# Kernel optimization log

Hardware: AMD Instinct MI355X
Metric: run time of the kernel (lower is better)

Reference implementation:

```python
import jax, jax.numpy as jnp
import numpy as np

H = 512
V = 50000
S = 400
B = 64


def setup_inputs() -> dict:
    key = jax.random.key(0)
    ks = jax.random.split(key, 20)
    inp = {
        'input': jax.random.normal(ks[0], (1, B, H), jnp.float32),
        'encoder_states': jax.random.normal(ks[1], (S, B, H), jnp.float32),
        'oov_enc_mask': jax.random.randint(ks[2], (S, B), 0, 2, jnp.int32),
        'hidden': jnp.zeros((1, B, H), jnp.float32),
        # GRU params (PyTorch layout: gates ordered r, z, n)
        'W_ih': jax.random.normal(ks[3], (3 * H, H), jnp.float32) * 0.02,
        'W_hh': jax.random.normal(ks[4], (3 * H, H), jnp.float32) * 0.02,
        'b_ih': jax.random.normal(ks[5], (3 * H,), jnp.float32) * 0.02,
        'b_hh': jax.random.normal(ks[6], (3 * H,), jnp.float32) * 0.02,
        # output vocab projection Linear(2H, V)
        'out_W': jax.random.normal(ks[7], (V, 2 * H), jnp.float32) * 0.02,
        'out_b': jax.random.normal(ks[8], (V,), jnp.float32) * 0.02,
        # additive attention params
        'v': jax.random.normal(ks[9], (H, 1), jnp.float32) * 0.02,
        'Wh': jax.random.normal(ks[10], (H, H), jnp.float32) * 0.02,
        'Ws': jax.random.normal(ks[11], (H, H), jnp.float32) * 0.02,
        'b_attn': jax.random.normal(ks[12], (1, H), jnp.float32) * 0.02,
        # pointer probability Linears (H -> 1)
        'pWh': jax.random.normal(ks[13], (1, H), jnp.float32) * 0.02,
        'pWs': jax.random.normal(ks[14], (1, H), jnp.float32) * 0.02,
        'pWx': jax.random.normal(ks[15], (1, H), jnp.float32) * 0.02,
        'pWx_b': jax.random.normal(ks[16], (1,), jnp.float32) * 0.02,
    }
    return inp


def reference(input, encoder_states, oov_enc_mask, hidden,
              W_ih, W_hh, b_ih, b_hh, out_W, out_b,
              v, Wh, Ws, b_attn, pWh, pWs, pWx, pWx_b):
    x = input[0]            # (B, H)
    h0 = hidden[0]          # (B, H)

    # --- single-step GRU (PyTorch gate order r, z, n) ---
    gi = x @ W_ih.T + b_ih      # (B, 3H)
    gh = h0 @ W_hh.T + b_hh     # (B, 3H)
    ir, iz, inn = jnp.split(gi, 3, axis=1)
    hr, hz, hn = jnp.split(gh, 3, axis=1)
    r = jax.nn.sigmoid(ir + hr)
    z = jax.nn.sigmoid(iz + hz)
    n = jnp.tanh(inn + r * hn)
    h = (1.0 - z) * n + z * h0          # decoder_state, (B, H)
    hidden_new = h[None]                # (1, B, H)

    # --- Bahdanau additive attention, softmax over seq axis ---
    x1 = jnp.einsum('sbh,hk->sbk', encoder_states, Wh)   # (S, B, H)
    x2 = h @ Ws                                          # (B, H) broadcasts over S
    scores = jnp.squeeze(jnp.tanh(x1 + x2 + b_attn) @ v, 2)  # (S, B)
    attn = jax.nn.softmax(scores, axis=0)                # (S, B)
    attn_bs = attn.T                                     # (B, S)

    context = jnp.einsum('bs,sbh->bh', attn_bs, encoder_states)  # (B, H)
    global_state = jnp.concatenate([h, context], axis=1)         # (B, 2H)

    # --- pointer probability ---
    p = jax.nn.sigmoid(context @ pWh.T + h @ pWs.T + x @ pWx.T + pWx_b)  # (B, 1)

    vocab_distr = p * jax.nn.selu(global_state @ out_W.T + out_b)        # (B, V)
    oov_vocab_distr = (1.0 - p) * (attn_bs * oov_enc_mask.astype(jnp.float32).T)  # (B, S)
    extended_vocab_distr = jnp.concatenate([vocab_distr, oov_vocab_distr], axis=1)

    return extended_vocab_distr, hidden_new, jnp.squeeze(p), attn
```

## Files before the change

kernel.cpp:

```cpp
#include <hip/hip_runtime.h>
#include <cmath>

#define H    512
#define H2   1024
#define V    50000
#define SEQ  400
#define EXT  (V + SEQ)
#define NB_V 782

typedef __attribute__((ext_vector_type(8))) short short8;
typedef __attribute__((ext_vector_type(4))) float floatx4;

__device__ __forceinline__ unsigned int bfpack2(float lo, float hi) {
    unsigned int a = __float_as_uint(lo) + 0x8000u;
    unsigned int b = __float_as_uint(hi) + 0x8000u;
    return __builtin_amdgcn_perm(b, a, 0x07060302);
}
__device__ __forceinline__ uint4 pack8(float4 a, float4 b) {
    uint4 r;
    r.x = bfpack2(a.x, a.y);
    r.y = bfpack2(a.z, a.w);
    r.z = bfpack2(b.x, b.y);
    r.w = bfpack2(b.z, b.w);
    return r;
}
__device__ __forceinline__ float4 ld4(const float* p) { return *(const float4*)p; }

__global__ __launch_bounds__(256) void k01_fused(
    const float* __restrict__ x, const float* __restrict__ h0,
    const float* __restrict__ W_ih, const float* __restrict__ W_hh,
    float* __restrict__ gacc,
    const float* __restrict__ Wh, const float* __restrict__ Ws,
    unsigned short* __restrict__ WhT, unsigned short* __restrict__ WsT)
{
    __shared__ __align__(16) unsigned char smem[65536];
    const int tid = threadIdx.x;

    if (blockIdx.x >= 64) {
        float (*T)[65] = (float (*)[65])smem;
        const int e   = blockIdx.x - 64;
        const int zz  = e >> 6, rem = e & 63;
        const int k0  = (rem & 7) * 64, n0 = (rem >> 3) * 64;
        const float* src = zz ? Ws : Wh;
        unsigned short* dst = zz ? WsT : WhT;
        #pragma unroll
        for (int i = 0; i < 16; ++i) {
            int ee = i * 256 + tid;
            int r = ee >> 6, c = ee & 63;
            T[r][c] = src[(size_t)(k0 + r) * H + n0 + c];
        }
        __syncthreads();
        #pragma unroll
        for (int i = 0; i < 16; ++i) {
            int ee = i * 256 + tid;
            int nn = ee >> 6, kk = ee & 63;
            unsigned int u = __float_as_uint(T[kk][nn]) + 0x8000u;
            dst[(size_t)(n0 + nn) * H + k0 + kk] = (unsigned short)(u >> 16);
        }
        return;
    }

    uint4* Ax = (uint4*)smem;
    uint4* Ah = (uint4*)(smem + 8192);
    uint4 (*Bg)[512] = (uint4 (*)[512])(smem + 16384);
    const int wave = tid >> 6, lane = tid & 63;
    const int lrow = lane & 15, q = lane >> 4;
    const int jb = blockIdx.x & 7, ks = blockIdx.x >> 3;
    const int J0 = jb * 64;
    const int kc = ks * 64;

    #pragma unroll
    for (int c = 0; c < 2; ++c) {
        int idx = c * 256 + tid;
        int m = idx >> 3, j2 = idx & 7, k8 = j2 ^ (m & 7);
        const float* sx = x  + m * H + kc + k8 * 8;
        const float* sh = h0 + m * H + kc + k8 * 8;
        Ax[idx] = pack8(ld4(sx), ld4(sx + 4));
        Ah[idx] = pack8(ld4(sh), ld4(sh + 4));
    }
    #pragma unroll
    for (int g = 0; g < 6; ++g) {
        const float* Wb = (g < 3) ? W_ih : W_hh;
        const int go = (g % 3) * H;
        #pragma unroll
        for (int c = 0; c < 2; ++c) {
            int idx = c * 256 + tid;
            int n = idx >> 3, j2 = idx & 7, k8 = j2 ^ (n & 7);
            const float* sw = Wb + (size_t)(go + J0 + n) * H + kc + k8 * 8;
            Bg[g][idx] = pack8(ld4(sw), ld4(sw + 4));
        }
    }
    __syncthreads();

    floatx4 accm[6][4];
    #pragma unroll
    for (int g = 0; g < 6; ++g)
        #pragma unroll
        for (int mt = 0; mt < 4; ++mt) accm[g][mt] = (floatx4){0.f, 0.f, 0.f, 0.f};

    #pragma unroll
    for (int kk8 = 0; kk8 < 8; kk8 += 4) {
        const int k8 = kk8 + q;
        short8 ax[4], ah[4];
        #pragma unroll
        for (int mt = 0; mt < 4; ++mt) {
            int m = mt * 16 + lrow;
            ax[mt] = *(const short8*)&Ax[m * 8 + (k8 ^ (m & 7))];
            ah[mt] = *(const short8*)&Ah[m * 8 + (k8 ^ (m & 7))];
        }
        const int n = wave * 16 + lrow;
        const int gidx = n * 8 + (k8 ^ (n & 7));
        #pragma unroll
        for (int g = 0; g < 6; ++g) {
            short8 bb = *(const short8*)&Bg[g][gidx];
            #pragma unroll
            for (int mt = 0; mt < 4; ++mt)
                accm[g][mt] = __builtin_amdgcn_mfma_f32_16x16x32_bf16(
                    (g < 3) ? ax[mt] : ah[mt], bb, accm[g][mt], 0, 0, 0);
        }
    }
    const int j = J0 + wave * 16 + lrow;
    #pragma unroll
    for (int g = 0; g < 6; ++g)
        #pragma unroll
        for (int mt = 0; mt < 4; ++mt)
            #pragma unroll
            for (int r = 0; r < 4; ++r) {
                const int bb = mt * 16 + q * 4 + r;
                gacc[(((size_t)g * 8 + ks) * 64 + bb) * H + j] = accm[g][mt][r];
            }
}

__global__ __launch_bounds__(256) void k1_gru_fin(
    const float* __restrict__ gacc, const float* __restrict__ h0,
    const float* __restrict__ b_ih, const float* __restrict__ b_hh,
    float* __restrict__ h_out)
{
    const int e = blockIdx.x * 256 + threadIdx.x;
    const int j = e & (H - 1);
    const int b = e >> 9;
    float gs[6];
    #pragma unroll
    for (int g = 0; g < 6; ++g) {
        float sum = 0.f;
        #pragma unroll
        for (int ks = 0; ks < 8; ++ks)
            sum += gacc[(((size_t)g * 8 + ks) * 64 + b) * H + j];
        gs[g] = sum;
    }
    float rg = 1.f / (1.f + expf(-(gs[0] + b_ih[j] + gs[3] + b_hh[j])));
    float zg = 1.f / (1.f + expf(-(gs[1] + b_ih[H + j] + gs[4] + b_hh[H + j])));
    float ng = tanhf(gs[2] + b_ih[2 * H + j] + rg * (gs[5] + b_hh[2 * H + j]));
    float h0v = h0[b * H + j];
    h_out[b * H + j] = (1.f - zg) * ng + zg * h0v;
}

__global__ __launch_bounds__(256) void k2_x2(
    const float* __restrict__ h, const unsigned short* __restrict__ WsT,
    const float* __restrict__ b_attn, float* __restrict__ x2)
{
    __shared__ uint4 Ag[512];
    __shared__ uint4 Bgg[512];
    const int tid  = threadIdx.x;
    const int wave = tid >> 6, lane = tid & 63;
    const int lrow = lane & 15, q = lane >> 4;
    const int n0   = blockIdx.x * 64;

    floatx4 acc[4];
    #pragma unroll
    for (int mt = 0; mt < 4; ++mt) acc[mt] = (floatx4){0.f, 0.f, 0.f, 0.f};

    for (int kc = 0; kc < H; kc += 64) {
        __syncthreads();
        #pragma unroll
        for (int c = 0; c < 2; ++c) {
            int idx = c * 256 + tid;
            int m = idx >> 3, j2 = idx & 7, k8 = j2 ^ (m & 7);
            const float* sh = h + m * H + kc + k8 * 8;
            Ag[idx] = pack8(ld4(sh), ld4(sh + 4));
            Bgg[idx] = *(const uint4*)(WsT + (size_t)(n0 + m) * H + kc + k8 * 8);
        }
        __syncthreads();
        #pragma unroll
        for (int kk8 = 0; kk8 < 8; kk8 += 4) {
            const int k8 = kk8 + q;
            const int n = wave * 16 + lrow;
            short8 bb = *(const short8*)&Bgg[n * 8 + (k8 ^ (n & 7))];
            #pragma unroll
            for (int mt = 0; mt < 4; ++mt) {
                int m = mt * 16 + lrow;
                short8 a = *(const short8*)&Ag[m * 8 + (k8 ^ (m & 7))];
                acc[mt] = __builtin_amdgcn_mfma_f32_16x16x32_bf16(a, bb, acc[mt], 0, 0, 0);
            }
        }
    }
    const int n = n0 + wave * 16 + lrow;
    const float ba = b_attn[n];
    #pragma unroll
    for (int mt = 0; mt < 4; ++mt)
        #pragma unroll
        for (int r = 0; r < 4; ++r) {
            const int bb = mt * 16 + q * 4 + r;
            x2[bb * H + n] = acc[mt][r] + ba;
        }
}

__global__ __launch_bounds__(256) void k3_scores(
    const float* __restrict__ enc, const unsigned short* __restrict__ WhT,
    const float* __restrict__ x2, const float* __restrict__ v,
    float* __restrict__ part)
{
    __shared__ uint4 AsG[512];
    __shared__ uint4 BsG[2048];
    __shared__ float red[256];
    const int s   = blockIdx.x;
    const int nc  = blockIdx.y;
    const int n0  = nc * 256;
    const int tid  = threadIdx.x;
    const int wave = tid >> 6, lane = tid & 63;
    const int lrow = lane & 15, q = lane >> 4;

    floatx4 acc[4][4];
    #pragma unroll
    for (int mt = 0; mt < 4; ++mt)
        #pragma unroll
        for (int nt = 0; nt < 4; ++nt) acc[mt][nt] = (floatx4){0.f, 0.f, 0.f, 0.f};

    const float* Abase = enc + (size_t)s * 64 * H;
    for (int kc = 0; kc < H; kc += 64) {
        __syncthreads();
        #pragma unroll
        for (int c = 0; c < 2; ++c) {
            int idx = c * 256 + tid;
            int m = idx >> 3, k8 = (idx & 7) ^ (m & 7);
            const float* sa = Abase + m * H + kc + k8 * 8;
            AsG[idx] = pack8(ld4(sa), ld4(sa + 4));
        }
        #pragma unroll
        for (int c = 0; c < 8; ++c) {
            int idx = c * 256 + tid;
            int n = idx >> 3, k8 = (idx & 7) ^ (n & 7);
            BsG[idx] = *(const uint4*)(WhT + (size_t)(n0 + n) * H + kc + k8 * 8);
        }
        __syncthreads();
        #pragma unroll
        for (int kk8 = 0; kk8 < 8; kk8 += 4) {
            const int k8 = kk8 + q;
            short8 a[4], b[4];
            #pragma unroll
            for (int mt = 0; mt < 4; ++mt) {
                int m = mt * 16 + lrow;
                a[mt] = *(const short8*)&AsG[m * 8 + (k8 ^ (m & 7))];
            }
            #pragma unroll
            for (int nt = 0; nt < 4; ++nt) {
                int n = wave * 64 + nt * 16 + lrow;
                b[nt] = *(const short8*)&BsG[n * 8 + (k8 ^ (n & 7))];
            }
            #pragma unroll
            for (int mt = 0; mt < 4; ++mt)
                #pragma unroll
                for (int nt = 0; nt < 4; ++nt)
                    acc[mt][nt] = __builtin_amdgcn_mfma_f32_16x16x32_bf16(
                        a[mt], b[nt], acc[mt][nt], 0, 0, 0);
        }
    }
    float val[4][4];
    #pragma unroll
    for (int mt = 0; mt < 4; ++mt) {
        #pragma unroll
        for (int r = 0; r < 4; ++r) {
            const int bb = mt * 16 + q * 4 + r;
            float sum = 0.f;
            #pragma unroll
            for (int nt = 0; nt < 4; ++nt) {
                const int n = n0 + wave * 64 + nt * 16 + lrow;
                sum += tanhf(acc[mt][nt][r] + x2[bb * H + n]) * v[n];
            }
            #pragma unroll
            for (int off = 8; off > 0; off >>= 1) sum += __shfl_down(sum, off, 16);
            val[mt][r] = sum;
        }
    }
    __syncthreads();
    if (lrow == 0) {
        #pragma unroll
        for (int mt = 0; mt < 4; ++mt)
            #pragma unroll
            for (int r = 0; r < 4; ++r)
                red[wave * 64 + mt * 16 + q * 4 + r] = val[mt][r];
    }
    __syncthreads();
    if (tid < 64) {
        float sc = red[tid] + red[64 + tid] + red[128 + tid] + red[192 + tid];
        part[((size_t)nc * SEQ + s) * 64 + tid] = sc;
    }
}

__global__ __launch_bounds__(512) void k4_softmax(
    const float* __restrict__ part, float* __restrict__ attn_out)
{
    const int b = blockIdx.x;
    const int t = threadIdx.x;
    __shared__ float red[8];
    __shared__ float smax, ssum;
    float myv = 0.f, val = -1e30f;
    if (t < SEQ) {
        myv = part[(size_t)t * 64 + b]
            + part[((size_t)SEQ + t) * 64 + b];
        val = myv;
    }
    float m = val;
    #pragma unroll
    for (int off = 32; off > 0; off >>= 1) m = fmaxf(m, __shfl_down(m, off, 64));
    if ((t & 63) == 0) red[t >> 6] = m;
    __syncthreads();
    if (t == 0) {
        float mm = red[0];
        #pragma unroll
        for (int w = 1; w < 8; ++w) mm = fmaxf(mm, red[w]);
        smax = mm;
    }
    __syncthreads();
    float e = (t < SEQ) ? expf(myv - smax) : 0.f;
    float ssv = e;
    #pragma unroll
    for (int off = 32; off > 0; off >>= 1) ssv += __shfl_down(ssv, off, 64);
    if ((t & 63) == 0) red[t >> 6] = ssv;
    __syncthreads();
    if (t == 0) {
        float ss = 0.f;
        #pragma unroll
        for (int w = 0; w < 8; ++w) ss += red[w];
        ssum = ss;
    }
    __syncthreads();
    if (t < SEQ) attn_out[t * 64 + b] = e / ssum;
}

__global__ __launch_bounds__(128) void k5_context(
    const float* __restrict__ enc, const float* __restrict__ attn,
    float* __restrict__ ctxp)
{
    const int b  = blockIdx.x;
    const int hc = blockIdx.y;
    const int sg = blockIdx.z;
    const int t  = threadIdx.x;
    __shared__ float a_s[100];
    if (t < 100) a_s[t] = attn[(sg * 100 + t) * 64 + b];
    __syncthreads();
    const int hh = hc * 128 + t;
    const float* p = enc + ((size_t)(sg * 100) * 64 + b) * H + hh;
    float a0 = 0.f, a1 = 0.f;
    #pragma unroll 5
    for (int i = 0; i < 100; i += 2) {
        a0 += a_s[i]     * p[0];
        a1 += a_s[i + 1] * p[(size_t)64 * H];
        p += (size_t)128 * H;
    }
    ctxp[((size_t)sg * 64 + b) * H + hh] = a0 + a1;
}

__global__ __launch_bounds__(512) void k5b_p(
    const float* __restrict__ ctxp, const float* __restrict__ pWh,
    const float* __restrict__ hdec, const float* __restrict__ pWs,
    const float* __restrict__ x, const float* __restrict__ pWx,
    const float* __restrict__ pWx_b,
    float* __restrict__ p_out, float* __restrict__ p_ws,
    unsigned short* __restrict__ gsb)
{
    const int b = blockIdx.x;
    const int t = threadIdx.x;
    __shared__ float rbuf[8];
    float c = ctxp[((size_t)0 * 64 + b) * H + t]
            + ctxp[((size_t)1 * 64 + b) * H + t]
            + ctxp[((size_t)2 * 64 + b) * H + t]
            + ctxp[((size_t)3 * 64 + b) * H + t];
    float hv = hdec[b * H + t];
    gsb[(size_t)b * H2 + t]     = (unsigned short)((__float_as_uint(hv) + 0x8000u) >> 16);
    gsb[(size_t)b * H2 + H + t] = (unsigned short)((__float_as_uint(c)  + 0x8000u) >> 16);
    float term = c * pWh[t] + hv * pWs[t] + x[b * H + t] * pWx[t];
    #pragma unroll
    for (int off = 32; off > 0; off >>= 1) term += __shfl_down(term, off, 64);
    if ((t & 63) == 0) rbuf[t >> 6] = term;
    __syncthreads();
    if (t == 0) {
        float ssv = pWx_b[0];
        #pragma unroll
        for (int w = 0; w < 8; ++w) ssv += rbuf[w];
        float pv = 1.f / (1.f + expf(-ssv));
        p_out[b] = pv;
        p_ws[b]  = pv;
    }
}

__global__ __launch_bounds__(256) void k6_vocab(
    const unsigned short* __restrict__ gsb, const float* __restrict__ outW,
    const float* __restrict__ outb, const float* __restrict__ p_ws,
    const float* __restrict__ attn, const int* __restrict__ mask,
    float* __restrict__ ext)
{
    const int tid = threadIdx.x;
    if (blockIdx.x >= NB_V) {
        int e = (blockIdx.x - NB_V) * 256 + tid;
        int s = e >> 6, b = e & 63;
        float val = (1.f - p_ws[b]) * attn[e] * (mask[e] ? 1.f : 0.f);
        ext[(size_t)b * EXT + V + s] = val;
        return;
    }
    __shared__ uint4 AsG[512];
    __shared__ uint4 BsG[512];
    __shared__ float p_l[64];
    const int wave = tid >> 6, lane = tid & 63;
    const int lrow = lane & 15, q = lane >> 4;
    const int v0   = blockIdx.x * 64;

    if (tid < 64) p_l[tid] = p_ws[tid];

    floatx4 acc[4];
    #pragma unroll
    for (int mt = 0; mt < 4; ++mt) acc[mt] = (floatx4){0.f, 0.f, 0.f, 0.f};

    for (int kc = 0; kc < H2; kc += 64) {
        __syncthreads();
        #pragma unroll
        for (int c = 0; c < 2; ++c) {
            int idx = c * 256 + tid;
            int m = idx >> 3, k8 = (idx & 7) ^ (m & 7);
            AsG[idx] = *(const uint4*)(gsb + (size_t)m * H2 + kc + k8 * 8);
        }
        #pragma unroll
        for (int c = 0; c < 2; ++c) {
            int idx = c * 256 + tid;
            int n = idx >> 3, k8 = (idx & 7) ^ (n & 7);
            int vr = v0 + n; if (vr >= V) vr = V - 1;
            const float* sb = outW + (size_t)vr * H2 + kc + k8 * 8;
            BsG[idx] = pack8(ld4(sb), ld4(sb + 4));
        }
        __syncthreads();
        #pragma unroll
        for (int kk8 = 0; kk8 < 8; kk8 += 4) {
            const int k8 = kk8 + q;
            const int n = wave * 16 + lrow;
            short8 bb = *(const short8*)&BsG[n * 8 + (k8 ^ (n & 7))];
            #pragma unroll
            for (int mt = 0; mt < 4; ++mt) {
                int m = mt * 16 + lrow;
                short8 a = *(const short8*)&AsG[m * 8 + (k8 ^ (m & 7))];
                acc[mt] = __builtin_amdgcn_mfma_f32_16x16x32_bf16(a, bb, acc[mt], 0, 0, 0);
            }
        }
    }
    const int n = v0 + wave * 16 + lrow;
    if (n < V) {
        const float ob = outb[n];
        #pragma unroll
        for (int mt = 0; mt < 4; ++mt) {
            #pragma unroll
            for (int r = 0; r < 4; ++r) {
                const int bb = mt * 16 + q * 4 + r;
                float zz = acc[mt][r] + ob;
                float sv = (zz > 0.f) ? 1.0507009873554805f * zz
                                      : 1.7580993408473766f * (expf(zz) - 1.f);
                ext[(size_t)bb * EXT + n] = p_l[bb] * sv;
            }
        }
    }
}

extern "C" void kernel_launch(void* const* d_in, const int* in_sizes, int n_in,
                              void* d_out, int out_size, void* d_ws, size_t ws_size,
                              hipStream_t stream)
{
    (void)in_sizes; (void)n_in; (void)out_size; (void)ws_size;
    const float* x      = (const float*)d_in[0];
    const float* enc    = (const float*)d_in[1];
    const int*   mask   = (const int*)  d_in[2];
    const float* h0     = (const float*)d_in[3];
    const float* W_ih   = (const float*)d_in[4];
    const float* W_hh   = (const float*)d_in[5];
    const float* b_ih   = (const float*)d_in[6];
    const float* b_hh   = (const float*)d_in[7];
    const float* outW   = (const float*)d_in[8];
    const float* outb   = (const float*)d_in[9];
    const float* v      = (const float*)d_in[10];
    const float* Wh     = (const float*)d_in[11];
    const float* Ws     = (const float*)d_in[12];
    const float* b_attn = (const float*)d_in[13];
    const float* pWh    = (const float*)d_in[14];
    const float* pWs    = (const float*)d_in[15];
    const float* pWx    = (const float*)d_in[16];
    const float* pWx_b  = (const float*)d_in[17];

    float* out        = (float*)d_out;
    float* out_ext    = out;
    float* out_hidden = out + (size_t)64 * EXT;
    float* out_p      = out_hidden + 64 * H;
    float* out_attn   = out_p + 64;

    float* ws       = (float*)d_ws;
    float* ws_x2    = ws;
    float* ws_part  = ws_x2 + 64 * H;
    float* ws_ctxp  = ws_part + 4 * SEQ * 64;
    float* ws_ctx   = ws_ctxp + 4 * 64 * H;
    float* ws_p     = ws_ctx + 64 * H;
    float* ws_gacc  = ws_p + 64;
    unsigned short* ws_whT = (unsigned short*)(ws_gacc + 6 * 8 * 64 * H);
    unsigned short* ws_wsT = ws_whT + (size_t)H * H;
    unsigned short* ws_gsb = ws_wsT + (size_t)H * H;

    k01_fused<<<192, 256, 0, stream>>>(x, h0, W_ih, W_hh, ws_gacc,
                                       Wh, Ws, ws_whT, ws_wsT);
    k1_gru_fin<<<128, 256, 0, stream>>>(ws_gacc, h0, b_ih, b_hh, out_hidden);
    k2_x2<<<8, 256, 0, stream>>>(out_hidden, ws_wsT, b_attn, ws_x2);
    k3_scores<<<dim3(SEQ, 2), 256, 0, stream>>>(enc, ws_whT, ws_x2, v, ws_part);
    k4_softmax<<<64, 512, 0, stream>>>(ws_part, out_attn);
    k5_context<<<dim3(64, 4, 4), 128, 0, stream>>>(enc, out_attn, ws_ctxp);
    k5b_p<<<64, 512, 0, stream>>>(ws_ctxp, pWh, out_hidden, pWs, x, pWx, pWx_b,
                                  out_p, ws_p, ws_gsb);
    k6_vocab<<<NB_V + 100, 256, 0, stream>>>(ws_gsb, outW, outb, ws_p,
                                             out_attn, mask, out_ext);
}
```

Before: 463.2 us.

## Fuse softmax into context kernel and vectorize encoder reads with float4

Merges the softmax and context kernels into one launch, with each block recomputing the per-batch softmax over all 400 positions redundantly, then reducing a 50-position slice of encoder states. Context accumulation now uses float4 loads, with each thread covering 4 hidden elements, and splits S into 8 chunks instead of 4. This removes one kernel launch and the round trip of attention weights through global memory. The cost is duplicated softmax work across the 8 sequence groups and a larger partial-sum buffer for the next kernel to read.

```diff
diff --git a/kernel.cpp b/kernel.cpp
--- a/kernel.cpp
+++ b/kernel.cpp
@@ -297,68 +297,75 @@
     }
 }
 
-__global__ __launch_bounds__(512) void k4_softmax(
-    const float* __restrict__ part, float* __restrict__ attn_out)
-{
-    const int b = blockIdx.x;
-    const int t = threadIdx.x;
-    __shared__ float red[8];
+__global__ __launch_bounds__(128) void k45_ctx(
+    const float* __restrict__ part, const float* __restrict__ enc,
+    float* __restrict__ attn_out, float* __restrict__ ctxp)
+{
+    const int b  = blockIdx.x;
+    const int sg = blockIdx.y;
+    const int t  = threadIdx.x;
+    __shared__ float a_all[SEQ];
+    __shared__ float red2[2];
     __shared__ float smax, ssum;
-    float myv = 0.f, val = -1e30f;
-    if (t < SEQ) {
-        myv = part[(size_t)t * 64 + b]
-            + part[((size_t)SEQ + t) * 64 + b];
-        val = myv;
-    }
-    float m = val;
-    #pragma unroll
-    for (int off = 32; off > 0; off >>= 1) m = fmaxf(m, __shfl_down(m, off, 64));
-    if ((t & 63) == 0) red[t >> 6] = m;
-    __syncthreads();
-    if (t == 0) {
-        float mm = red[0];
-        #pragma unroll
-        for (int w = 1; w < 8; ++w) mm = fmaxf(mm, red[w]);
-        smax = mm;
-    }
-    __syncthreads();
-    float e = (t < SEQ) ? expf(myv - smax) : 0.f;
-    float ssv = e;
-    #pragma unroll
-    for (int off = 32; off > 0; off >>= 1) ssv += __shfl_down(ssv, off, 64);
-    if ((t & 63) == 0) red[t >> 6] = ssv;
-    __syncthreads();
-    if (t == 0) {
-        float ss = 0.f;
-        #pragma unroll
-        for (int w = 0; w < 8; ++w) ss += red[w];
-        ssum = ss;
-    }
-    __syncthreads();
-    if (t < SEQ) attn_out[t * 64 + b] = e / ssum;
-}
-
-__global__ __launch_bounds__(128) void k5_context(
-    const float* __restrict__ enc, const float* __restrict__ attn,
-    float* __restrict__ ctxp)
-{
-    const int b  = blockIdx.x;
-    const int hc = blockIdx.y;
-    const int sg = blockIdx.z;
-    const int t  = threadIdx.x;
-    __shared__ float a_s[100];
-    if (t < 100) a_s[t] = attn[(sg * 100 + t) * 64 + b];
-    __syncthreads();
-    const int hh = hc * 128 + t;
-    const float* p = enc + ((size_t)(sg * 100) * 64 + b) * H + hh;
-    float a0 = 0.f, a1 = 0.f;
+
+    float mv[4];
+    float mx = -1e30f;
+    #pragma unroll
+    for (int i = 0; i < 4; ++i) {
+        int s = i * 128 + t;
+        if (s < SEQ) {
+            float vv = part[(size_t)s * 64 + b] + part[((size_t)SEQ + s) * 64 + b];
+            mv[i] = vv;
+            mx = fmaxf(mx, vv);
+        }
+    }
+    #pragma unroll
+    for (int off = 32; off > 0; off >>= 1) mx = fmaxf(mx, __shfl_down(mx, off, 64));
+    if ((t & 63) == 0) red2[t >> 6] = mx;
+    __syncthreads();
+    if (t == 0) smax = fmaxf(red2[0], red2[1]);
+    __syncthreads();
+    float ev[4];
+    float se = 0.f;
+    #pragma unroll
+    for (int i = 0; i < 4; ++i) {
+        int s = i * 128 + t;
+        if (s < SEQ) { ev[i] = expf(mv[i] - smax); se += ev[i]; }
+    }
+    #pragma unroll
+    for (int off = 32; off > 0; off >>= 1) se += __shfl_down(se, off, 64);
+    if ((t & 63) == 0) red2[t >> 6] = se;
+    __syncthreads();
+    if (t == 0) ssum = red2[0] + red2[1];
+    __syncthreads();
+    const float inv = 1.f / ssum;
+    #pragma unroll
+    for (int i = 0; i < 4; ++i) {
+        int s = i * 128 + t;
+        if (s < SEQ) {
+            float av = ev[i] * inv;
+            a_all[s] = av;
+            if (sg == 0) attn_out[s * 64 + b] = av;
+        }
+    }
+    __syncthreads();
+
+    const int hh = 4 * t;
+    const float* p = enc + ((size_t)(sg * 50) * 64 + b) * H + hh;
+    float4 a0 = {0.f, 0.f, 0.f, 0.f}, a1 = {0.f, 0.f, 0.f, 0.f};
     #pragma unroll 5
-    for (int i = 0; i < 100; i += 2) {
-        a0 += a_s[i]     * p[0];
-        a1 += a_s[i + 1] * p[(size_t)64 * H];
+    for (int i = 0; i < 50; i += 2) {
+        float4 e0 = *(const float4*)p;
+        float4 e1 = *(const float4*)(p + (size_t)64 * H);
+        float w0 = a_all[sg * 50 + i];
+        float w1 = a_all[sg * 50 + i + 1];
+        a0.x += w0 * e0.x; a0.y += w0 * e0.y; a0.z += w0 * e0.z; a0.w += w0 * e0.w;
+        a1.x += w1 * e1.x; a1.y += w1 * e1.y; a1.z += w1 * e1.z; a1.w += w1 * e1.w;
         p += (size_t)128 * H;
     }
-    ctxp[((size_t)sg * 64 + b) * H + hh] = a0 + a1;
+    float4 r;
+    r.x = a0.x + a1.x; r.y = a0.y + a1.y; r.z = a0.z + a1.z; r.w = a0.w + a1.w;
+    *(float4*)&ctxp[((size_t)sg * 64 + b) * H + hh] = r;
 }
 
 __global__ __launch_bounds__(512) void k5b_p(
@@ -372,10 +379,10 @@
     const int b = blockIdx.x;
     const int t = threadIdx.x;
     __shared__ float rbuf[8];
-    float c = ctxp[((size_t)0 * 64 + b) * H + t]
-            + ctxp[((size_t)1 * 64 + b) * H + t]
-            + ctxp[((size_t)2 * 64 + b) * H + t]
-            + ctxp[((size_t)3 * 64 + b) * H + t];
+    float c = 0.f;
+    #pragma unroll
+    for (int sg = 0; sg < 8; ++sg)
+        c += ctxp[((size_t)sg * 64 + b) * H + t];
     float hv = hdec[b * H + t];
     gsb[(size_t)b * H2 + t]     = (unsigned short)((__float_as_uint(hv) + 0x8000u) >> 16);
     gsb[(size_t)b * H2 + H + t] = (unsigned short)((__float_as_uint(c)  + 0x8000u) >> 16);
@@ -502,8 +509,7 @@
     float* ws_x2    = ws;
     float* ws_part  = ws_x2 + 64 * H;
     float* ws_ctxp  = ws_part + 4 * SEQ * 64;
-    float* ws_ctx   = ws_ctxp + 4 * 64 * H;
-    float* ws_p     = ws_ctx + 64 * H;
+    float* ws_p     = ws_ctxp + 8 * 64 * H;
     float* ws_gacc  = ws_p + 64;
     unsigned short* ws_whT = (unsigned short*)(ws_gacc + 6 * 8 * 64 * H);
     unsigned short* ws_wsT = ws_whT + (size_t)H * H;
@@ -514,8 +520,7 @@
     k1_gru_fin<<<128, 256, 0, stream>>>(ws_gacc, h0, b_ih, b_hh, out_hidden);
     k2_x2<<<8, 256, 0, stream>>>(out_hidden, ws_wsT, b_attn, ws_x2);
     k3_scores<<<dim3(SEQ, 2), 256, 0, stream>>>(enc, ws_whT, ws_x2, v, ws_part);
-    k4_softmax<<<64, 512, 0, stream>>>(ws_part, out_attn);
-    k5_context<<<dim3(64, 4, 4), 128, 0, stream>>>(enc, out_attn, ws_ctxp);
+    k45_ctx<<<dim3(64, 8), 128, 0, stream>>>(ws_part, enc, out_attn, ws_ctxp);
     k5b_p<<<64, 512, 0, stream>>>(ws_ctxp, pWh, out_hidden, pWs, x, pWx, pWx_b,
                                   out_p, ws_p, ws_gsb);
     k6_vocab<<<NB_V + 100, 256, 0, stream>>>(ws_gsb, outW, outb, ws_p,
```

Result: faster. 448.7 us, median of 2 (-3.1%).
